# Kernel optimization log

Measured on AMD Instinct MI355X. Metric: run time of the kernel, lower is better.

## Reference

```python
import jax, jax.numpy as jnp
import numpy as np

D_FEAT = 6
T = 64
HID = 128
N = 8192
EPS = 1e-5


def setup_inputs() -> dict:
    key = jax.random.key(0)
    ks = jax.random.split(key, 16)
    s = 0.08
    rn = lambda k, shape: jax.random.normal(k, shape, dtype=jnp.float32) * s
    return {
        "x": jax.random.normal(ks[0], (N, D_FEAT * T), dtype=jnp.float32),
        "w_ih0": rn(ks[1], (3 * HID, D_FEAT)),
        "w_hh0": rn(ks[2], (3 * HID, HID)),
        "b_ih0": rn(ks[3], (3 * HID,)),
        "b_hh0": rn(ks[4], (3 * HID,)),
        "w_ih1": rn(ks[5], (3 * HID, HID)),
        "w_hh1": rn(ks[6], (3 * HID, HID)),
        "b_ih1": rn(ks[7], (3 * HID,)),
        "b_hh1": rn(ks[8], (3 * HID,)),
        "bn1_g": jnp.ones((HID,), jnp.float32),
        "bn1_b": jnp.zeros((HID,), jnp.float32),
        "fc_w": rn(ks[9], (HID, HID)),
        "fc_b": rn(ks[10], (HID,)),
        "bn2_g": jnp.ones((HID,), jnp.float32),
        "bn2_b": jnp.zeros((HID,), jnp.float32),
        "fco_w": rn(ks[11], (1, HID)),
        "fco_b": rn(ks[12], (1,)),
    }


def _gru_layer(xs, w_ih, w_hh, b_ih, b_hh):
    # xs: [T, N, in] -> per-step hidden states [T, N, H] (torch nn.GRU math)
    H = w_hh.shape[1]
    gi_all = jnp.einsum('tni,gi->tng', xs, w_ih) + b_ih  # precompute input gates [T,N,3H]

    def step(h, gi):
        gh = h @ w_hh.T + b_hh
        i_r, i_z, i_n = jnp.split(gi, 3, axis=1)
        h_r, h_z, h_n = jnp.split(gh, 3, axis=1)
        r = jax.nn.sigmoid(i_r + h_r)
        z = jax.nn.sigmoid(i_z + h_z)
        n = jnp.tanh(i_n + r * h_n)
        h_new = (1.0 - z) * n + z * h
        return h_new, h_new

    h0 = jnp.zeros((xs.shape[1], H), dtype=xs.dtype)
    _, hs = jax.lax.scan(step, h0, gi_all)
    return hs


def _bn(x, g, b):
    # BatchNorm1d with track_running_stats=False: always uses batch stats
    mu = jnp.mean(x, axis=0)
    var = jnp.mean((x - mu) ** 2, axis=0)
    return (x - mu) * jax.lax.rsqrt(var + EPS) * g + b


def reference(x, w_ih0, w_hh0, b_ih0, b_hh0, w_ih1, w_hh1, b_ih1, b_hh1,
              bn1_g, bn1_b, fc_w, fc_b, bn2_g, bn2_b, fco_w, fco_b):
    n = x.shape[0]
    # reshape(N, d_feat, T).permute(0,2,1) -> time-major [T, N, d_feat] for scan
    xs = x.reshape(n, D_FEAT, T).transpose(2, 0, 1)
    h1 = _gru_layer(xs, w_ih0, w_hh0, b_ih0, b_hh0)
    h2 = _gru_layer(h1, w_ih1, w_hh1, b_ih1, b_hh1)
    hidden = _bn(h2[-1], bn1_g, bn1_b)  # [N, H]
    # cal_attention: mean_d(h_i * h_j) - mean(h_i)*mean(h_j)
    #   == (hidden @ hidden.T)/H - outer(row_means, row_means)  (exact identity)
    m = jnp.mean(hidden, axis=1)
    att = hidden @ hidden.T / jnp.float32(hidden.shape[1]) - jnp.outer(m, m)  # [N, N]
    out = att @ hidden              # [N, H]
    out = out @ fc_w.T + fc_b
    out = _bn(out, bn2_g, bn2_b)
    out = jax.nn.leaky_relu(out, 0.01)
    return (out @ fco_w.T + fco_b).squeeze(-1)  # [N]
```

## Files before the change

### kernel.cpp

```cpp
#include <hip/hip_runtime.h>

typedef unsigned short u16;
typedef short bf16x8 __attribute__((ext_vector_type(8)));
typedef float f32x4 __attribute__((ext_vector_type(4)));

#define NBATCH 8192

__device__ __forceinline__ f32x4 mfma16(bf16x8 a, bf16x8 b, f32x4 c) {
  return __builtin_amdgcn_mfma_f32_16x16x32_bf16(a, b, c, 0, 0, 0);
}
__device__ __forceinline__ u16 f2bf(float f) {
  unsigned int u = __float_as_uint(f);
  return (u16)((u + 0x7FFFu + ((u >> 16) & 1u)) >> 16);
}
__device__ __forceinline__ float bf2f(u16 h) {
  return __uint_as_float(((unsigned int)h) << 16);
}
__device__ __forceinline__ float sigm(float x) {
  return __builtin_amdgcn_rcpf(1.f + __builtin_amdgcn_exp2f(-1.44269504f * x));
}
__device__ __forceinline__ float tanh_(float x) {
  float t = __builtin_amdgcn_exp2f(2.88539008f * x);
  return 1.f - 2.f * __builtin_amdgcn_rcpf(t + 1.f);
}
__device__ __forceinline__ bf16x8 pack8(const float* p) {
  float4 a = *(const float4*)p, b = *(const float4*)(p + 4);
  bf16x8 r;
  r[0] = (short)f2bf(a.x); r[1] = (short)f2bf(a.y);
  r[2] = (short)f2bf(a.z); r[3] = (short)f2bf(a.w);
  r[4] = (short)f2bf(b.x); r[5] = (short)f2bf(b.y);
  r[6] = (short)f2bf(b.z); r[7] = (short)f2bf(b.w);
  return r;
}


#define A_WRZ  0
#define A_H0B  65536
#define A_XB   73728
#define A_LDS  75776

#define GRU0_STEP(RD, WR, T)                                                    \
  {                                                                             \
    if (xact && (T) < 63) {                                                     \
      u16 xh = f2bf(xv);                                                        \
      u16 xl = f2bf(xv - bf2f(xh));                                             \
      char* xw = sm + A_XB + (WR)*1024 + xm*64 + xd*2;                          \
      *(u16*)xw = xh; *(u16*)(xw + 16) = xl; *(u16*)(xw + 32) = xh;             \
      if ((T) < 62) xv = gx[(T) + 2];                                           \
    }                                                                           \
    f32x4 accr = {brzr, brzr, brzr, brzr};                                      \
    f32x4 accz = {brzz, brzz, brzz, brzz};                                      \
    f32x4 acch = {bhn0, bhn0, bhn0, bhn0};                                      \
    f32x4 acci = {bin0, bin0, bin0, bin0};                                      \
    _Pragma("unroll") for (int ki = 0; ki < 4; ++ki) {                          \
      bf16x8 a0 = *(bf16x8*)(sm + A_H0B + (RD)*4096 + arow0 + ad[ki]);          \
      bf16x8 br = *(bf16x8*)(sm + A_WRZ + browr + ad[ki]);                      \
      bf16x8 bz = *(bf16x8*)(sm + A_WRZ + browz + ad[ki]);                      \
      accr = mfma16(a0, br, accr);                                              \
      accz = mfma16(a0, bz, accz);                                              \
      acch = mfma16(a0, wn0[ki], acch);                                         \
    }                                                                           \
    {                                                                           \
      bf16x8 ax0 = *(bf16x8*)(sm + A_XB + (RD)*1024 + xr0);                     \
      accr = mfma16(ax0, wf0a, accr);                                           \
      accz = mfma16(ax0, wf0b, accz);                                           \
      acci = mfma16(ax0, wf0c, acci);                                           \
    }                                                                           \
    if ((T) >= 1) {       \
      uint2 gv = *(const uint2*)(sm + A_H0B + (RD)*4096 + tid*8);               \
      *(uint2*)(h0seq + (size_t)((T)-1)*2097152 + gofs) = gv;                   \
    }                                                                           \
    _Pragma("unroll") for (int r = 0; r < 4; ++r) {                             \
      float rr = sigm(accr[r]);                                                 \
      float zz = sigm(accz[r]);                                                 \
      float nn = tanh_(__builtin_fmaf(rr, acch[r], acci[r]));                   \
      float h = h0s[r]; h = __builtin_fmaf(zz, h - nn, nn); h0s[r] = h;         \
      *(u16*)(sm + A_H0B + (WR)*4096 + st[r]) = f2bf(h);                        \
    }                                                                           \
    __syncthreads();                                                            \
  }

__global__ __attribute__((amdgpu_flat_work_group_size(512, 512)))
void k_gru0(const float* __restrict__ x,
            const float* __restrict__ wih0, const float* __restrict__ whh0,
            const float* __restrict__ bih0, const float* __restrict__ bhh0,
            char* __restrict__ h0seq) {
  extern __shared__ char sm[];
  const int tid = threadIdx.x;
  const int wid = tid >> 6;
  const int lane = tid & 63;
  const int lq = lane >> 4;
  const int ul = lane & 15;
  const int u  = wid * 16 + ul;
  const int n0 = blockIdx.x * 16;
  const int sx = (ul & 7) << 4;
  const int gofs = blockIdx.x * 4096 + tid * 8;

  for (int idx = tid; idx < 2560; idx += 512)
    *(float*)(sm + A_H0B + idx * 4) = 0.f;
  for (int idx = tid; idx < 8192; idx += 512) {
    int g = idx >> 5, c4 = (idx & 31) * 4;
    float4 v = *(const float4*)(whh0 + g * 128 + c4);
    unsigned int p0 = (unsigned int)f2bf(v.x) | ((unsigned int)f2bf(v.y) << 16);
    unsigned int p1 = (unsigned int)f2bf(v.z) | ((unsigned int)f2bf(v.w) << 16);
    unsigned int* dst = (unsigned int*)(sm + A_WRZ + g * 256 + ((c4 * 2) ^ ((g & 7) << 4)));
    dst[0] = p0; dst[1] = p1;
  }
  bf16x8 wn0[4];
#pragma unroll
  for (int ki = 0; ki < 4; ++ki)
    wn0[ki] = pack8(whh0 + (256 + u) * 128 + ki * 32 + lq * 8);

  bf16x8 wf0a, wf0b, wf0c;
  {
    u16 t0[8] = {0,0,0,0,0,0,0,0}, t1[8] = {0,0,0,0,0,0,0,0}, t2[8] = {0,0,0,0,0,0,0,0};
    u16* ts[3] = {t0, t1, t2};
#pragma unroll
    for (int i = 0; i < 3; ++i) {
      int g = u + 128 * i;
      if (lq < 2) {
        for (int d = 0; d < 6; ++d) ts[i][d] = f2bf(wih0[g * 6 + d]);
      } else if (lq == 2) {
        for (int d = 0; d < 6; ++d) {
          float w = wih0[g * 6 + d];
          u16 h = f2bf(w);
          ts[i][d] = f2bf(w - bf2f(h));
        }
      }
    }
    wf0a = *(bf16x8*)t0; wf0b = *(bf16x8*)t1; wf0c = *(bf16x8*)t2;
  }
  const float brzr = bih0[u] + bhh0[u];
  const float brzz = bih0[u + 128] + bhh0[u + 128];
  const float bin0 = bih0[u + 256], bhn0 = bhh0[u + 256];

  int ad[4];
#pragma unroll
  for (int ki = 0; ki < 4; ++ki) ad[ki] = (ki * 64 + lq * 16) ^ sx;
  const int arow0 = ul * 256;
  const int xr0 = ul * 64 + lq * 16;
  const int browr = u * 256;
  const int browz = (u + 128) * 256;
  int st[4];
#pragma unroll
  for (int r = 0; r < 4; ++r) {
    int m = lq * 4 + r;
    st[r] = m * 256 + ((u * 2) ^ ((m & 7) << 4));
  }

  float h0s[4];
#pragma unroll
  for (int r = 0; r < 4; ++r) h0s[r] = 0.f;

  const int xm = tid / 6, xd = tid - 6 * xm;
  const bool xact = tid < 96;
  const float* gx = x + (size_t)(n0 + xm) * 384 + xd * 64;

  __syncthreads();

  float xv = 0.f;
  if (xact) {
    float x0 = gx[0];
    u16 h = f2bf(x0);
    u16 l = f2bf(x0 - bf2f(h));
    char* p = sm + A_XB + xm * 64 + xd * 2;
    *(u16*)p = h; *(u16*)(p + 16) = l; *(u16*)(p + 32) = h;
    xv = gx[1];
  }
  __syncthreads();

  for (int t = 0; t < 64; t += 2) {
    GRU0_STEP(0, 1, t)
    GRU0_STEP(1, 0, t + 1)
  }
  {
    uint2 gv = *(const uint2*)(sm + A_H0B + tid * 8);
    *(uint2*)(h0seq + (size_t)63 * 2097152 + gofs) = gv;
  }
}

#define B_WRZ  0
#define B_H0IN 65536
#define B_H1B  73728
#define B_LDS  77824

#define GRU1_STEP(P, T)                                                         \
  {                                                                             \
    uint2 hv = {0u, 0u};                                                        \
    if ((T) < 63) hv = *(const uint2*)(gsrc + (size_t)((T)+1)*2097152);         \
    f32x4 accr = {brzr, brzr, brzr, brzr};                                      \
    f32x4 accz = {brzz, brzz, brzz, brzz};                                      \
    f32x4 acci = {bin1, bin1, bin1, bin1};                                      \
    f32x4 acch = {bhn1, bhn1, bhn1, bhn1};                                      \
    _Pragma("unroll") for (int ki = 0; ki < 4; ++ki) {                          \
      bf16x8 p0 = *(bf16x8*)(sm + B_H0IN + (P)*4096 + arow0 + ad[ki]);          \
      bf16x8 q0 = *(bf16x8*)(sm + B_H1B + arow0 + ad[ki]);                      \
      bf16x8 br = *(bf16x8*)(sm + B_WRZ + browr + ad[ki]);                      \
      bf16x8 bz = *(bf16x8*)(sm + B_WRZ + browz + ad[ki]);                      \
      accr = mfma16(p0, wih1f[0][ki], accr);                                    \
      accr = mfma16(q0, br, accr);                                              \
      accz = mfma16(p0, wih1f[1][ki], accz);                                    \
      accz = mfma16(q0, bz, accz);                                              \
      acci = mfma16(p0, wih1f[2][ki], acci);                                    \
      acch = mfma16(q0, wn1[ki], acch);                                         \
    }                                                                           \
    u16 hw[4];                                                                  \
    _Pragma("unroll") for (int r = 0; r < 4; ++r) {                             \
      float rr = sigm(accr[r]);                                                 \
      float zz = sigm(accz[r]);                                                 \
      float nn = tanh_(__builtin_fmaf(rr, acch[r], acci[r]));                   \
      float h = h1s[r]; h = __builtin_fmaf(zz, h - nn, nn); h1s[r] = h;         \
      hw[r] = f2bf(h);                                                          \
    }                                                                           \
    __syncthreads();                 \
    if ((T) < 63) *(uint2*)(sm + B_H0IN + ((P)^1)*4096 + tid*8) = hv;           \
    _Pragma("unroll") for (int r = 0; r < 4; ++r)                               \
      *(u16*)(sm + B_H1B + st[r]) = hw[r];                                      \
    __syncthreads();                            \
  }

__global__ __attribute__((amdgpu_flat_work_group_size(512, 512)))
void k_gru1(const float* __restrict__ wih1, const float* __restrict__ whh1,
            const float* __restrict__ bih1, const float* __restrict__ bhh1,
            const char* __restrict__ h0seq, float* __restrict__ hraw) {
  extern __shared__ char sm[];
  const int tid = threadIdx.x;
  const int wid = tid >> 6;
  const int lane = tid & 63;
  const int lq = lane >> 4;
  const int ul = lane & 15;
  const int u  = wid * 16 + ul;
  const int n0 = blockIdx.x * 16;
  const int sx = (ul & 7) << 4;
  const char* gsrc = h0seq + blockIdx.x * 4096 + tid * 8;

  for (int idx = tid; idx < 1024; idx += 512)
    *(float*)(sm + B_H1B + idx * 4) = 0.f;
  for (int idx = tid; idx < 8192; idx += 512) {
    int g = idx >> 5, c4 = (idx & 31) * 4;
    float4 v = *(const float4*)(whh1 + g * 128 + c4);
    unsigned int p0 = (unsigned int)f2bf(v.x) | ((unsigned int)f2bf(v.y) << 16);
    unsigned int p1 = (unsigned int)f2bf(v.z) | ((unsigned int)f2bf(v.w) << 16);
    unsigned int* dst = (unsigned int*)(sm + B_WRZ + g * 256 + ((c4 * 2) ^ ((g & 7) << 4)));
    dst[0] = p0; dst[1] = p1;
  }
  {
    uint2 h0v = *(const uint2*)(gsrc);
    *(uint2*)(sm + B_H0IN + tid * 8) = h0v;
  }
  bf16x8 wih1f[3][4], wn1[4];
#pragma unroll
  for (int i = 0; i < 3; ++i) {
    int g = u + 128 * i;
#pragma unroll
    for (int ki = 0; ki < 4; ++ki)
      wih1f[i][ki] = pack8(wih1 + g * 128 + ki * 32 + lq * 8);
  }
#pragma unroll
  for (int ki = 0; ki < 4; ++ki)
    wn1[ki] = pack8(whh1 + (256 + u) * 128 + ki * 32 + lq * 8);

  const float brzr = bih1[u] + bhh1[u];
  const float brzz = bih1[u + 128] + bhh1[u + 128];
  const float bin1 = bih1[u + 256], bhn1 = bhh1[u + 256];

  int ad[4];
#pragma unroll
  for (int ki = 0; ki < 4; ++ki) ad[ki] = (ki * 64 + lq * 16) ^ sx;
  const int arow0 = ul * 256;
  const int browr = u * 256;
  const int browz = (u + 128) * 256;
  int st[4];
#pragma unroll
  for (int r = 0; r < 4; ++r) {
    int m = lq * 4 + r;
    st[r] = m * 256 + ((u * 2) ^ ((m & 7) << 4));
  }

  float h1s[4];
#pragma unroll
  for (int r = 0; r < 4; ++r) h1s[r] = 0.f;

  __syncthreads();

  for (int t = 0; t < 64; t += 2) {
    GRU1_STEP(0, t)
    GRU1_STEP(1, t + 1)
  }

#pragma unroll
  for (int r = 0; r < 4; ++r) {
    int m = lq * 4 + r;
    hraw[(size_t)(n0 + m) * 128 + u] = h1s[r];
  }
}

__global__ void k_bn1p(const float* __restrict__ hraw, float* __restrict__ p) {
  __shared__ float s0[256], s1[256];
  int tid = threadIdx.x, b = blockIdx.x;
  int f = tid & 127, r = tid >> 7;
  float s = 0.f, q = 0.f;
  for (int n = b * 64 + r; n < b * 64 + 64; n += 2) {
    float v = hraw[(size_t)n * 128 + f];
    s += v; q += v * v;
  }
  s0[tid] = s; s1[tid] = q;
  __syncthreads();
  if (tid < 128) {
    p[b * 256 + tid] = s0[tid] + s0[tid + 128];
    p[b * 256 + 128 + tid] = s1[tid] + s1[tid + 128];
  }
}

__global__ void k_bn1r(const float* __restrict__ p, float* __restrict__ mu1,
                       float* __restrict__ rs1) {
  int f = threadIdx.x;
  float s = 0.f, q = 0.f;
  for (int b = 0; b < 128; ++b) { s += p[b * 256 + f]; q += p[b * 256 + 128 + f]; }
  float mu = s / 8192.f, var = q / 8192.f - mu * mu;
  mu1[f] = mu; rs1[f] = rsqrtf(var + 1e-5f);
}

__global__ void k_attp(const float* __restrict__ hraw, const float* __restrict__ mu1,
                       const float* __restrict__ rs1, const float* __restrict__ g1,
                       const float* __restrict__ b1, float* __restrict__ hidden,
                       float* __restrict__ mvec, float* __restrict__ gpart,
                       float* __restrict__ mhpart) {
  __shared__ float hid[64][128];
  __shared__ float mld[64];
  int tid = threadIdx.x, blk = blockIdx.x, n0 = blk * 64;
  for (int idx = tid; idx < 64 * 128; idx += 256) {
    int n = idx >> 7, f = idx & 127;
    float v = (hraw[(size_t)(n0 + n) * 128 + f] - mu1[f]) * rs1[f] * g1[f] + b1[f];
    hid[n][f] = v;
    hidden[(size_t)(n0 + n) * 128 + f] = v;
  }
  __syncthreads();
  if (tid < 64) {
    float s = 0.f;
    for (int f = 0; f < 128; ++f) s += hid[tid][f];
    s *= (1.f / 128.f);
    mld[tid] = s; mvec[n0 + tid] = s;
  }
  __syncthreads();
  int i = tid >> 1, j0 = (tid & 1) * 64;
  float acc[64];
#pragma unroll
  for (int j = 0; j < 64; ++j) acc[j] = 0.f;
  for (int n = 0; n < 64; ++n) {
    float a = hid[n][i];
#pragma unroll
    for (int j = 0; j < 64; ++j) acc[j] += a * hid[n][j0 + j];
  }
#pragma unroll
  for (int j = 0; j < 64; ++j) gpart[(size_t)blk * 16384 + i * 128 + j0 + j] = acc[j];
  if (tid < 128) {
    float s = 0.f;
    for (int n = 0; n < 64; ++n) s += mld[n] * hid[n][tid];
    mhpart[blk * 128 + tid] = s;
  }
}

__global__ void k_attfa(const float* __restrict__ gpart, const float* __restrict__ mhpart,
                        float* __restrict__ gfull, float* __restrict__ mhfull) {
  int idx = blockIdx.x * 256 + threadIdx.x;
  float s = 0.f;
  for (int b = 0; b < 128; ++b) s += gpart[(size_t)b * 16384 + idx];
  gfull[idx] = s;
  if (blockIdx.x == 0 && threadIdx.x < 128) {
    float t = 0.f;
    for (int b = 0; b < 128; ++b) t += mhpart[b * 128 + threadIdx.x];
    mhfull[threadIdx.x] = t;
  }
}

__global__ void k_attfb(const float* __restrict__ gfull, const float* __restrict__ mhfull,
                        const float* __restrict__ fcw, float* __restrict__ m2,
                        float* __restrict__ uvec) {
  int idx = blockIdx.x * 128 + threadIdx.x;
  int k = idx >> 7, j = idx & 127;
  const float4* ga = (const float4*)(gfull + k * 128);
  const float4* fb = (const float4*)(fcw + j * 128);
  float a0 = 0.f, a1 = 0.f, a2 = 0.f, a3 = 0.f;
#pragma unroll 8
  for (int f = 0; f < 32; ++f) {
    float4 a = ga[f], b = fb[f];
    a0 += a.x * b.x; a1 += a.y * b.y; a2 += a.z * b.z; a3 += a.w * b.w;
  }
  m2[idx] = (a0 + a1 + a2 + a3) * (1.f / 128.f);
  if (idx < 128) {
    float s = 0.f;
    const float* fr = fcw + idx * 128;
#pragma unroll 8
    for (int f = 0; f < 128; ++f) s += mhfull[f] * fr[f];
    uvec[idx] = s;
  }
}

__global__ void k_out2(const float* __restrict__ hidden, const float* __restrict__ mvec,
                       const float* __restrict__ m2g, const float* __restrict__ uvec,
                       const float* __restrict__ fcb, float* __restrict__ out2,
                       float* __restrict__ bn2p) {
  extern __shared__ char smo[];
  float* m2l = (float*)smo;
  float* hl = m2l + 16384;
  float* ml = hl + 4096;
  float* red = ml + 32;
  int tid = threadIdx.x, blk = blockIdx.x, n0 = blk * 32;
  for (int idx = tid; idx < 16384; idx += 256) m2l[idx] = m2g[idx];
  for (int idx = tid; idx < 4096; idx += 256) hl[idx] = hidden[(size_t)n0 * 128 + idx];
  if (tid < 32) ml[tid] = mvec[n0 + tid];
  __syncthreads();
  int j = tid & 127, rg = tid >> 7;
  float uj = uvec[j], bj = fcb[j];
  float s1 = 0.f, s2 = 0.f;
  for (int q = 0; q < 16; ++q) {
    int nl = rg * 16 + q;
    float s = bj - ml[nl] * uj;
    const float* hr = hl + nl * 128;
#pragma unroll 8
    for (int k = 0; k < 128; ++k) s += hr[k] * m2l[k * 128 + j];
    out2[(size_t)(n0 + nl) * 128 + j] = s;
    s1 += s; s2 += s * s;
  }
  red[tid] = s1; red[256 + tid] = s2;
  __syncthreads();
  if (tid < 128) {
    bn2p[blk * 256 + tid] = red[tid] + red[128 + tid];
    bn2p[blk * 256 + 128 + tid] = red[256 + tid] + red[384 + tid];
  }
}

__global__ void k_bn2(const float* __restrict__ bn2p, float* __restrict__ mu2,
                      float* __restrict__ rs2) {
  int j = threadIdx.x;
  float s = 0.f, q = 0.f;
  for (int b = 0; b < 256; ++b) {
    s += bn2p[b * 256 + j];
    q += bn2p[b * 256 + 128 + j];
  }
  float mu = s / 8192.f, var = q / 8192.f - mu * mu;
  mu2[j] = mu; rs2[j] = rsqrtf(var + 1e-5f);
}

__global__ void k_fin(const float* __restrict__ out2, const float* __restrict__ mu2,
                      const float* __restrict__ rs2, const float* __restrict__ g2,
                      const float* __restrict__ b2, const float* __restrict__ fcow,
                      const float* __restrict__ fcob, float* __restrict__ y) {
  int tid = threadIdx.x, lane = tid & 63, w = tid >> 6;
  int n = blockIdx.x * 4 + w;
  float s = 0.f;
#pragma unroll
  for (int h = 0; h < 2; ++h) {
    int j = lane + h * 64;
    float v = (out2[(size_t)n * 128 + j] - mu2[j]) * rs2[j] * g2[j] + b2[j];
    v = fmaxf(v, 0.01f * v);
    s += v * fcow[j];
  }
  for (int off = 32; off; off >>= 1) s += __shfl_down(s, off);
  if (!lane) y[n] = s + fcob[0];
}

extern "C" void kernel_launch(void* const* d_in, const int* in_sizes, int n_in,
                              void* d_out, int out_size, void* d_ws, size_t ws_size,
                              hipStream_t stream) {
  const float* x    = (const float*)d_in[0];
  const float* wih0 = (const float*)d_in[1];
  const float* whh0 = (const float*)d_in[2];
  const float* bih0 = (const float*)d_in[3];
  const float* bhh0 = (const float*)d_in[4];
  const float* wih1 = (const float*)d_in[5];
  const float* whh1 = (const float*)d_in[6];
  const float* bih1 = (const float*)d_in[7];
  const float* bhh1 = (const float*)d_in[8];
  const float* g1   = (const float*)d_in[9];
  const float* b1   = (const float*)d_in[10];
  const float* fcw  = (const float*)d_in[11];
  const float* fcb  = (const float*)d_in[12];
  const float* g2   = (const float*)d_in[13];
  const float* b2   = (const float*)d_in[14];
  const float* fcow = (const float*)d_in[15];
  const float* fcob = (const float*)d_in[16];

  char* ws = (char*)d_ws;
  float* hraw   = (float*)(ws + 0);
  float* hidden = (float*)(ws + 4194304);
  float* mvec   = (float*)(ws + 8388608);
  float* mu1    = (float*)(ws + 8421376);
  float* rs1    = (float*)(ws + 8421888);
  float* gpart  = (float*)(ws + 8422400);
  float* mhpart = (float*)(ws + 16811008);
  float* m2     = (float*)(ws + 16876544);
  float* uvec   = (float*)(ws + 16942080);
  float* out2   = (float*)(ws + 16942592);
  float* bn2p   = (float*)(ws + 21136896);
  float* mu2    = (float*)(ws + 21399040);
  float* rs2    = (float*)(ws + 21399552);
  float* gfull  = (float*)(ws + 21400064);
  float* mhfull = (float*)(ws + 21465600);
  char*  h0seq  = (char*)(ws + 21495808);

  (void)hipFuncSetAttribute((const void*)k_gru0,
                            hipFuncAttributeMaxDynamicSharedMemorySize, A_LDS);
  (void)hipFuncSetAttribute((const void*)k_gru1,
                            hipFuncAttributeMaxDynamicSharedMemorySize, B_LDS);
  (void)hipFuncSetAttribute((const void*)k_out2,
                            hipFuncAttributeMaxDynamicSharedMemorySize, 84096);

  k_gru0<<<512, 512, A_LDS, stream>>>(x, wih0, whh0, bih0, bhh0, h0seq);
  k_gru1<<<512, 512, B_LDS, stream>>>(wih1, whh1, bih1, bhh1, h0seq, hraw);
  k_bn1p<<<128, 256, 0, stream>>>(hraw, bn2p);
  k_bn1r<<<1, 128, 0, stream>>>(bn2p, mu1, rs1);
  k_attp<<<128, 256, 0, stream>>>(hraw, mu1, rs1, g1, b1, hidden, mvec, gpart, mhpart);
  k_attfa<<<64, 256, 0, stream>>>(gpart, mhpart, gfull, mhfull);
  k_attfb<<<128, 128, 0, stream>>>(gfull, mhfull, fcw, m2, uvec);
  k_out2<<<256, 256, 84096, stream>>>(hidden, mvec, m2, uvec, fcb, out2, bn2p);
  k_bn2<<<1, 128, 0, stream>>>(bn2p, mu2, rs2);
  k_fin<<<2048, 256, 0, stream>>>(out2, mu2, rs2, g2, b2, fcow, fcob, (float*)d_out);
}
```

Baseline: 342.5 us.

## Keep recurrent r/z weights in registers and double-buffer GRU1 hidden state

Both GRU kernels now hold the r and z recurrent weight fragments in VGPRs instead of staging them in LDS. This removes two LDS reads per MFMA step and cuts LDS use from about 75KB to 10-16KB, which could allow more blocks per CU. GRU1 also double-buffers the h1 state so each step needs one barrier instead of two. The cost is much higher register pressure, especially in GRU1 with 24 weight fragments, which risks spills or lower occupancy.

Result: faster. 329.2 us (-3.9%).

```diff
diff --git a/kernel.cpp b/kernel.cpp
--- a/kernel.cpp
+++ b/kernel.cpp
@@ -34,10 +34,9 @@
 }
 
 
-#define A_WRZ  0
-#define A_H0B  65536
-#define A_XB   73728
-#define A_LDS  75776
+#define A_H0B  0
+#define A_XB   8192
+#define A_LDS  10240
 
 #define GRU0_STEP(RD, WR, T)                                                    \
   {                                                                             \
@@ -54,10 +53,8 @@
     f32x4 acci = {bin0, bin0, bin0, bin0};                                      \
     _Pragma("unroll") for (int ki = 0; ki < 4; ++ki) {                          \
       bf16x8 a0 = *(bf16x8*)(sm + A_H0B + (RD)*4096 + arow0 + ad[ki]);          \
-      bf16x8 br = *(bf16x8*)(sm + A_WRZ + browr + ad[ki]);                      \
-      bf16x8 bz = *(bf16x8*)(sm + A_WRZ + browz + ad[ki]);                      \
-      accr = mfma16(a0, br, accr);                                              \
-      accz = mfma16(a0, bz, accz);                                              \
+      accr = mfma16(a0, wr0[ki], accr);                                         \
+      accz = mfma16(a0, wz0[ki], accz);                                         \
       acch = mfma16(a0, wn0[ki], acch);                                         \
     }                                                                           \
     {                                                                           \
@@ -98,18 +95,14 @@
 
   for (int idx = tid; idx < 2560; idx += 512)
     *(float*)(sm + A_H0B + idx * 4) = 0.f;
-  for (int idx = tid; idx < 8192; idx += 512) {
-    int g = idx >> 5, c4 = (idx & 31) * 4;
-    float4 v = *(const float4*)(whh0 + g * 128 + c4);
-    unsigned int p0 = (unsigned int)f2bf(v.x) | ((unsigned int)f2bf(v.y) << 16);
-    unsigned int p1 = (unsigned int)f2bf(v.z) | ((unsigned int)f2bf(v.w) << 16);
-    unsigned int* dst = (unsigned int*)(sm + A_WRZ + g * 256 + ((c4 * 2) ^ ((g & 7) << 4)));
-    dst[0] = p0; dst[1] = p1;
-  }
-  bf16x8 wn0[4];
-#pragma unroll
-  for (int ki = 0; ki < 4; ++ki)
+
+  bf16x8 wr0[4], wz0[4], wn0[4];
+#pragma unroll
+  for (int ki = 0; ki < 4; ++ki) {
+    wr0[ki] = pack8(whh0 + u * 128 + ki * 32 + lq * 8);
+    wz0[ki] = pack8(whh0 + (128 + u) * 128 + ki * 32 + lq * 8);
     wn0[ki] = pack8(whh0 + (256 + u) * 128 + ki * 32 + lq * 8);
+  }
 
   bf16x8 wf0a, wf0b, wf0c;
   {
@@ -139,8 +132,6 @@
   for (int ki = 0; ki < 4; ++ki) ad[ki] = (ki * 64 + lq * 16) ^ sx;
   const int arow0 = ul * 256;
   const int xr0 = ul * 64 + lq * 16;
-  const int browr = u * 256;
-  const int browz = (u + 128) * 256;
   int st[4];
 #pragma unroll
   for (int r = 0; r < 4; ++r) {
@@ -179,12 +170,11 @@
   }
 }
 
-#define B_WRZ  0
-#define B_H0IN 65536
-#define B_H1B  73728
-#define B_LDS  77824
-
-#define GRU1_STEP(P, T)                                                         \
+#define B_H0IN 0
+#define B_H1B  8192
+#define B_LDS  16384
+
+#define GRU1_STEP(RD, WR, T)                                                    \
   {                                                                             \
     uint2 hv = {0u, 0u};                                                        \
     if ((T) < 63) hv = *(const uint2*)(gsrc + (size_t)((T)+1)*2097152);         \
@@ -193,30 +183,24 @@
     f32x4 acci = {bin1, bin1, bin1, bin1};                                      \
     f32x4 acch = {bhn1, bhn1, bhn1, bhn1};                                      \
     _Pragma("unroll") for (int ki = 0; ki < 4; ++ki) {                          \
-      bf16x8 p0 = *(bf16x8*)(sm + B_H0IN + (P)*4096 + arow0 + ad[ki]);          \
-      bf16x8 q0 = *(bf16x8*)(sm + B_H1B + arow0 + ad[ki]);                      \
-      bf16x8 br = *(bf16x8*)(sm + B_WRZ + browr + ad[ki]);                      \
-      bf16x8 bz = *(bf16x8*)(sm + B_WRZ + browz + ad[ki]);                      \
+      bf16x8 p0 = *(bf16x8*)(sm + B_H0IN + (RD)*4096 + arow0 + ad[ki]);         \
+      bf16x8 q0 = *(bf16x8*)(sm + B_H1B + (RD)*4096 + arow0 + ad[ki]);          \
       accr = mfma16(p0, wih1f[0][ki], accr);                                    \
-      accr = mfma16(q0, br, accr);                                              \
+      accr = mfma16(q0, wr1[ki], accr);                                         \
       accz = mfma16(p0, wih1f[1][ki], accz);                                    \
-      accz = mfma16(q0, bz, accz);                                              \
+      accz = mfma16(q0, wz1[ki], accz);                                         \
       acci = mfma16(p0, wih1f[2][ki], acci);                                    \
       acch = mfma16(q0, wn1[ki], acch);                                         \
     }                                                                           \
-    u16 hw[4];                                                                  \
+    if ((T) < 63) *(uint2*)(sm + B_H0IN + (WR)*4096 + tid*8) = hv;              \
     _Pragma("unroll") for (int r = 0; r < 4; ++r) {                             \
       float rr = sigm(accr[r]);                                                 \
       float zz = sigm(accz[r]);                                                 \
       float nn = tanh_(__builtin_fmaf(rr, acch[r], acci[r]));                   \
       float h = h1s[r]; h = __builtin_fmaf(zz, h - nn, nn); h1s[r] = h;         \
-      hw[r] = f2bf(h);                                                          \
-    }                                                                           \
-    __syncthreads();                 \
-    if ((T) < 63) *(uint2*)(sm + B_H0IN + ((P)^1)*4096 + tid*8) = hv;           \
-    _Pragma("unroll") for (int r = 0; r < 4; ++r)                               \
-      *(u16*)(sm + B_H1B + st[r]) = hw[r];                                      \
-    __syncthreads();                            \
+      *(u16*)(sm + B_H1B + (WR)*4096 + st[r]) = f2bf(h);                        \
+    }                                                                           \
+    __syncthreads();                                                            \
   }
 
 __global__ __attribute__((amdgpu_flat_work_group_size(512, 512)))
@@ -236,19 +220,11 @@
 
   for (int idx = tid; idx < 1024; idx += 512)
     *(float*)(sm + B_H1B + idx * 4) = 0.f;
-  for (int idx = tid; idx < 8192; idx += 512) {
-    int g = idx >> 5, c4 = (idx & 31) * 4;
-    float4 v = *(const float4*)(whh1 + g * 128 + c4);
-    unsigned int p0 = (unsigned int)f2bf(v.x) | ((unsigned int)f2bf(v.y) << 16);
-    unsigned int p1 = (unsigned int)f2bf(v.z) | ((unsigned int)f2bf(v.w) << 16);
-    unsigned int* dst = (unsigned int*)(sm + B_WRZ + g * 256 + ((c4 * 2) ^ ((g & 7) << 4)));
-    dst[0] = p0; dst[1] = p1;
-  }
   {
     uint2 h0v = *(const uint2*)(gsrc);
     *(uint2*)(sm + B_H0IN + tid * 8) = h0v;
   }
-  bf16x8 wih1f[3][4], wn1[4];
+  bf16x8 wih1f[3][4], wr1[4], wz1[4], wn1[4];
 #pragma unroll
   for (int i = 0; i < 3; ++i) {
     int g = u + 128 * i;
@@ -257,8 +233,11 @@
       wih1f[i][ki] = pack8(wih1 + g * 128 + ki * 32 + lq * 8);
   }
 #pragma unroll
-  for (int ki = 0; ki < 4; ++ki)
+  for (int ki = 0; ki < 4; ++ki) {
+    wr1[ki] = pack8(whh1 + u * 128 + ki * 32 + lq * 8);
+    wz1[ki] = pack8(whh1 + (128 + u) * 128 + ki * 32 + lq * 8);
     wn1[ki] = pack8(whh1 + (256 + u) * 128 + ki * 32 + lq * 8);
+  }
 
   const float brzr = bih1[u] + bhh1[u];
   const float brzz = bih1[u + 128] + bhh1[u + 128];
@@ -268,8 +247,6 @@
 #pragma unroll
   for (int ki = 0; ki < 4; ++ki) ad[ki] = (ki * 64 + lq * 16) ^ sx;
   const int arow0 = ul * 256;
-  const int browr = u * 256;
-  const int browz = (u + 128) * 256;
   int st[4];
 #pragma unroll
   for (int r = 0; r < 4; ++r) {
@@ -284,8 +261,8 @@
   __syncthreads();
 
   for (int t = 0; t < 64; t += 2) {
-    GRU1_STEP(0, t)
-    GRU1_STEP(1, t + 1)
+    GRU1_STEP(0, 1, t)
+    GRU1_STEP(1, 0, t + 1)
   }
 
 #pragma unroll
@@ -500,10 +477,6 @@
   float* mhfull = (float*)(ws + 21465600);
   char*  h0seq  = (char*)(ws + 21495808);
 
-  (void)hipFuncSetAttribute((const void*)k_gru0,
-                            hipFuncAttributeMaxDynamicSharedMemorySize, A_LDS);
-  (void)hipFuncSetAttribute((const void*)k_gru1,
-                            hipFuncAttributeMaxDynamicSharedMemorySize, B_LDS);
   (void)hipFuncSetAttribute((const void*)k_out2,
                             hipFuncAttributeMaxDynamicSharedMemorySize, 84096);
 
```
